# Performance work log

Hardware: AMD Instinct MI355X
Metric: run time of the kernel (lower is better)

## Reference

```python
import jax, jax.numpy as jnp
import numpy as np

N = 262144      # total nodes
E = 1048576     # total edges
G = 8192        # num graphs (= batch[-1]+1)
H = 128         # hidden
L = 4           # layers
VA = 64         # atom feature vocab
VB = 8          # bond feature vocab
FA = 9          # atom feature columns
FB = 3          # bond feature columns
BN_EPS = 1e-5


def _bn(x, g, b, m, v):
    # BatchNorm1d in eval mode: running stats
    return (x - m) * jax.lax.rsqrt(v + BN_EPS) * g + b


def setup_inputs() -> dict:
    key = jax.random.key(0)
    ks = jax.random.split(key, 40)
    rn = lambda k, s, sc=0.05: jax.random.normal(k, s, dtype=jnp.float32) * sc
    x = jax.random.randint(ks[0], (N, FA), 0, VA)
    edge_index = jax.random.randint(ks[1], (2, E), 0, N)
    edge_attr = jax.random.randint(ks[2], (E, FB), 0, VB)
    batch = jnp.sort(jax.random.randint(ks[3], (N,), 0, G))
    batch = batch.at[0].set(0).at[-1].set(G - 1)
    params = dict(
        atom_emb=rn(ks[4], (FA, VA, H)),
        vn_emb=rn(ks[5], (H,)),
        bond_emb=rn(ks[6], (L, FB, VB, H)),
        conv_eps=rn(ks[7], (L,)),
        conv_W1=rn(ks[8], (L, H, 2 * H)), conv_b1=rn(ks[9], (L, 2 * H)),
        conv_bn_g=1.0 + rn(ks[10], (L, 2 * H)), conv_bn_b=rn(ks[11], (L, 2 * H)),
        conv_bn_m=rn(ks[12], (L, 2 * H), 0.1),
        conv_bn_v=0.5 + jax.random.uniform(ks[13], (L, 2 * H)) * 0.5,
        conv_W2=rn(ks[14], (L, 2 * H, H)), conv_b2=rn(ks[15], (L, H)),
        vn1_W=rn(ks[16], (L, 2 * H, 2 * H)), vn1_b=rn(ks[17], (L, 2 * H)),
        vn1_g=1.0 + rn(ks[18], (L, 2 * H)), vn1_be=rn(ks[19], (L, 2 * H)),
        vn1_m=rn(ks[20], (L, 2 * H), 0.1),
        vn1_v=0.5 + jax.random.uniform(ks[21], (L, 2 * H)) * 0.5,
        vn2_W=rn(ks[22], (L, 2 * H, H)), vn2_b=rn(ks[23], (L, H)),
        vn2_g=1.0 + rn(ks[24], (L, H)), vn2_be=rn(ks[25], (L, H)),
        vn2_m=rn(ks[26], (L, H), 0.1),
        vn2_v=0.5 + jax.random.uniform(ks[27], (L, H)) * 0.5,
        pW1=rn(ks[28], (H, H)), pb1=rn(ks[29], (H,)),
        pW2=rn(ks[30], (H, 1)), pb2=rn(ks[31], (1,)),
    )
    return dict(x=x, edge_index=edge_index, edge_attr=edge_attr, batch=batch, **params)


def reference(x, edge_index, edge_attr, batch, atom_emb, vn_emb, bond_emb,
              conv_eps, conv_W1, conv_b1, conv_bn_g, conv_bn_b, conv_bn_m, conv_bn_v,
              conv_W2, conv_b2, vn1_W, vn1_b, vn1_g, vn1_be, vn1_m, vn1_v,
              vn2_W, vn2_b, vn2_g, vn2_be, vn2_m, vn2_v, pW1, pb1, pW2, pb2):
    src, dst = edge_index[0], edge_index[1]
    # AtomEncoder: sum of per-feature embeddings -> [N, H]
    h = atom_emb[jnp.arange(FA)[:, None], x.T].sum(0)
    # virtual node embedding broadcast to all graphs: [G, H]
    vn = jnp.broadcast_to(vn_emb, (G, H))
    for i in range(L):
        h = h + vn[batch]
        # CombConv (GIN-with-edge-features): msg = relu(x_j + bond_emb)
        e = bond_emb[i][jnp.arange(FB)[:, None], edge_attr.T].sum(0)  # [E, H]
        msg = jax.nn.relu(h[src] + e)
        agg = jax.ops.segment_sum(msg, dst, num_segments=N)  # [N, H]
        z = (1.0 + conv_eps[i]) * h + agg
        z = jax.nn.relu(_bn(z @ conv_W1[i] + conv_b1[i],
                            conv_bn_g[i], conv_bn_b[i], conv_bn_m[i], conv_bn_v[i]))
        h = z @ conv_W2[i] + conv_b2[i]
        # virtual node update: gather-concat-MLP, pool, MLP
        t = jnp.concatenate([vn[batch], h], axis=-1)  # [N, 2H]
        t = jax.nn.relu(_bn(t @ vn1_W[i] + vn1_b[i],
                            vn1_g[i], vn1_be[i], vn1_m[i], vn1_v[i]))
        pooled = jax.ops.segment_sum(t, batch, num_segments=G)  # [G, 2H]
        vn = jax.nn.relu(_bn(pooled @ vn2_W[i] + vn2_b[i],
                             vn2_g[i], vn2_be[i], vn2_m[i], vn2_v[i]))
    # JK='L': last virtual-node representation; dropout=0
    out = jax.nn.relu(vn @ pW1 + pb1) @ pW2 + pb2  # [G, 1]
    return jnp.clip(out, 0.0, 50.0)  # eval-mode clamp
```

## Files before the change

kernel.cpp:

```cpp
#include <hip/hip_runtime.h>
#include <hip/hip_fp16.h>

#define NN 262144
#define EE 1048576
#define GG 8192
#define HH 128
#define FBc 3
#define VAc 64
#define VBc 8
#define FAc 9

typedef _Float16 f16;
typedef _Float16 f16x8 __attribute__((ext_vector_type(8)));
typedef float f32x4 __attribute__((ext_vector_type(4)));

__device__ __forceinline__ float h2f(ushort u) {
    __half h; *(ushort*)&h = u; return __half2float(h);
}
__device__ __forceinline__ ushort f2h(float f) {
    __half h = __float2half_rn(f); return *(ushort*)&h;
}

__global__ void k_zero(float* __restrict__ p) {
    size_t i = (size_t)(blockIdx.x * 256 + threadIdx.x) * 4;
    *(float4*)(p + i) = make_float4(0.f, 0.f, 0.f, 0.f);
}

__global__ void k_atom(const int* __restrict__ x, const float* __restrict__ emb,
                       float* __restrict__ h) {
    int t = blockIdx.x * 256 + threadIdx.x;
    int n = t >> 5, c = (t & 31) << 2;
    if (n >= NN) return;
    float4 a = make_float4(0.f, 0.f, 0.f, 0.f);
#pragma unroll
    for (int f = 0; f < FAc; ++f) {
        int v = x[n * FAc + f];
        float4 e = *(const float4*)(emb + ((size_t)(f * VAc + v)) * HH + c);
        a.x += e.x; a.y += e.y; a.z += e.z; a.w += e.w;
    }
    *(float4*)(h + (size_t)n * HH + c) = a;
}

__global__ void k_init_vn(const float* __restrict__ vn_emb, float* __restrict__ vn) {
    int t = blockIdx.x * 256 + threadIdx.x;
    int g = t >> 5, c = (t & 31) << 2;
    *(float4*)(vn + (size_t)g * HH + c) = *(const float4*)(vn_emb + c);
}

__global__ void k_hist(const int* __restrict__ ei, int* __restrict__ deg) {
    int e = blockIdx.x * 256 + threadIdx.x;
    atomicAdd(&deg[ei[EE + e]], 1);
}
__global__ void k_scan1(const int* __restrict__ deg, int* __restrict__ rowptr,
                        int* __restrict__ sums) {
    __shared__ int s[256];
    int base = blockIdx.x * 1024 + threadIdx.x * 4;
    int4 d = *(const int4*)(deg + base);
    int t = d.x + d.y + d.z + d.w;
    s[threadIdx.x] = t;
    __syncthreads();
    for (int off = 1; off < 256; off <<= 1) {
        int v = (threadIdx.x >= off) ? s[threadIdx.x - off] : 0;
        __syncthreads();
        s[threadIdx.x] += v;
        __syncthreads();
    }
    int excl = s[threadIdx.x] - t;
    int4 o; o.x = excl; o.y = excl + d.x; o.z = o.y + d.y; o.w = o.z + d.z;
    *(int4*)(rowptr + base) = o;
    if (threadIdx.x == 255) sums[blockIdx.x] = s[255];
}
__global__ void k_scan2(int* __restrict__ sums) {
    __shared__ int s[256];
    int t = sums[threadIdx.x];
    s[threadIdx.x] = t;
    __syncthreads();
    for (int off = 1; off < 256; off <<= 1) {
        int v = (threadIdx.x >= off) ? s[threadIdx.x - off] : 0;
        __syncthreads();
        s[threadIdx.x] += v;
        __syncthreads();
    }
    sums[threadIdx.x] = s[threadIdx.x] - t;
}
__global__ void k_scan3(int* __restrict__ rowptr, const int* __restrict__ sums,
                        int* __restrict__ fill) {
    int base = blockIdx.x * 1024 + threadIdx.x * 4;
    int add = sums[blockIdx.x];
    int4 r = *(const int4*)(rowptr + base);
    r.x += add; r.y += add; r.z += add; r.w += add;
    *(int4*)(rowptr + base) = r;
    *(int4*)(fill + base) = r;
    if (blockIdx.x == 0 && threadIdx.x == 0) rowptr[NN] = EE;
}
__global__ void k_scatter(const int* __restrict__ ei, const int* __restrict__ ea,
                          int* __restrict__ fill, unsigned* __restrict__ packed) {
    int e = blockIdx.x * 256 + threadIdx.x;
    int dst = ei[EE + e];
    int pos = atomicAdd(&fill[dst], 1);
    unsigned cb = (unsigned)(ea[e * 3 + 0] + ea[e * 3 + 1] * 8 + ea[e * 3 + 2] * 64);
    packed[pos] = (unsigned)ei[e] | (cb << 18);
}

__global__ void k_ctab(const float* __restrict__ bemb, float* __restrict__ ctab) {
    int t = blockIdx.x * 256 + threadIdx.x;
    int cb = t >> 5, c = (t & 31) << 2;
    int a0 = cb & 7, a1 = (cb >> 3) & 7, a2 = cb >> 6;
    float4 b0 = *(const float4*)(bemb + (size_t)(0 * VBc + a0) * HH + c);
    float4 b1 = *(const float4*)(bemb + (size_t)(1 * VBc + a1) * HH + c);
    float4 b2 = *(const float4*)(bemb + (size_t)(2 * VBc + a2) * HH + c);
    float4 o = make_float4(b0.x + b1.x + b2.x, b0.y + b1.y + b2.y,
                           b0.z + b1.z + b2.z, b0.w + b1.w + b2.w);
    *(float4*)(ctab + (size_t)cb * HH + c) = o;
}

__global__ void k_wt(const float* __restrict__ W, ushort* __restrict__ Wt, int lk, int Nsrc) {
    int o = blockIdx.x * 256 + threadIdx.x;
    int K = 1 << lk;
    int c = o >> lk, k = o & (K - 1);
    Wt[o] = f2h(W[(size_t)k * Nsrc + c]);
}

__global__ void k_agg(const float* __restrict__ h, const float* __restrict__ vn,
                      const int* __restrict__ batch,
                      const int* __restrict__ rowptr, const unsigned* __restrict__ packed,
                      const float* __restrict__ ctab, ushort* __restrict__ agg) {
    int n = blockIdx.x * 4 + (threadIdx.x >> 6);
    int lane = threadIdx.x & 63;
    int co = lane * 2;
    int beg = rowptr[n], end = rowptr[n + 1];
    float a0 = 0.f, a1 = 0.f;
    int i = beg;
    for (; i + 1 < end; i += 2) {
        unsigned p0 = packed[i], p1 = packed[i + 1];
        int s0 = p0 & 0x3FFFF, s1 = p1 & 0x3FFFF;
        int c0 = p0 >> 18, c1 = p1 >> 18;
        float2 h0 = *(const float2*)(h + (size_t)s0 * HH + co);
        float2 h1 = *(const float2*)(h + (size_t)s1 * HH + co);
        float2 v0 = *(const float2*)(vn + (size_t)batch[s0] * HH + co);
        float2 v1 = *(const float2*)(vn + (size_t)batch[s1] * HH + co);
        float2 t0 = *(const float2*)(ctab + (size_t)c0 * HH + co);
        float2 t1 = *(const float2*)(ctab + (size_t)c1 * HH + co);
        a0 += fmaxf(h0.x + v0.x + t0.x, 0.f) + fmaxf(h1.x + v1.x + t1.x, 0.f);
        a1 += fmaxf(h0.y + v0.y + t0.y, 0.f) + fmaxf(h1.y + v1.y + t1.y, 0.f);
    }
    if (i < end) {
        unsigned p = packed[i];
        int src = p & 0x3FFFF, cb = p >> 18;
        float2 hv = *(const float2*)(h + (size_t)src * HH + co);
        float2 vv = *(const float2*)(vn + (size_t)batch[src] * HH + co);
        float2 ct = *(const float2*)(ctab + (size_t)cb * HH + co);
        a0 += fmaxf(hv.x + vv.x + ct.x, 0.f);
        a1 += fmaxf(hv.y + vv.y + ct.y, 0.f);
    }
    ushort2 o; o.x = f2h(a0 * 0.0625f); o.y = f2h(a1 * 0.0625f);
    *(ushort2*)(agg + (size_t)n * HH + co) = o;
}

__global__ void __launch_bounds__(512)
k_conv(float* __restrict__ hio, const ushort* __restrict__ agg,
       const ushort* __restrict__ W1t, const ushort* __restrict__ W2t,
       const ushort* __restrict__ W3t,
       const int* __restrict__ batch, const float* __restrict__ vn,
       const float* __restrict__ vnW,
       const float* __restrict__ eps_ptr, const float* __restrict__ b1,
       const float* __restrict__ g1v, const float* __restrict__ be1,
       const float* __restrict__ m1, const float* __restrict__ v1,
       const float* __restrict__ b2,
       const float* __restrict__ g3, const float* __restrict__ be3,
       const float* __restrict__ m3, const float* __restrict__ v3,
       float* __restrict__ pooled) {
    __shared__ ushort As[128][136];
    __shared__ ushort zs[128][264];
    __shared__ ushort Wb[128][136];
    __shared__ int batchL[128];
    float(*ts)[132] = (float(*)[132]) & zs[0][0];
    const int tid = threadIdx.x;
    const int r0 = blockIdx.x * 128;
    const int w = tid >> 6, l = tid & 63, lr = l & 15, lg = l >> 4;
    if (tid < 128) batchL[tid] = batch[r0 + tid];
    const float eps1 = 1.f + eps_ptr[0];
    __syncthreads();

    {
        int row = tid >> 2, q = tid & 3;
        const float* hp = hio + (size_t)(r0 + row) * HH + q * 32;
        const float* vp = vn + (size_t)batchL[row] * HH + q * 32;
        const ushort* ap = agg + (size_t)(r0 + row) * HH + q * 32;
#pragma unroll
        for (int j4 = 0; j4 < 4; ++j4) {
            f16x8 u = *(const f16x8*)(ap + j4 * 8);
            f16x8 o;
#pragma unroll
            for (int j = 0; j < 8; ++j) {
                float hv = hp[j4 * 8 + j] + vp[j4 * 8 + j];
                o[j] = (f16)(eps1 * hv * 0.0625f + (float)u[j]);
            }
            *(f16x8*)&As[row][q * 32 + j4 * 8] = o;
        }
    }

    for (int ch = 0; ch < 2; ++ch) {
        __syncthreads();
        {
            int c = tid >> 2, q = tid & 3;
            const ushort* wp = W1t + (size_t)(ch * 128 + c) * HH + q * 32;
#pragma unroll
            for (int j4 = 0; j4 < 4; ++j4)
                *(f16x8*)&Wb[c][q * 32 + j4 * 8] = *(const f16x8*)(wp + j4 * 8);
        }
        __syncthreads();
        f32x4 acc[8] = {};
#pragma unroll
        for (int k0 = 0; k0 < 128; k0 += 32) {
            f16x8 af = *(const f16x8*)&As[w * 16 + lr][k0 + lg * 8];
#pragma unroll
            for (int fc = 0; fc < 8; ++fc) {
                f16x8 bf = *(const f16x8*)&Wb[fc * 16 + lr][k0 + lg * 8];
                acc[fc] = __builtin_amdgcn_mfma_f32_16x16x32_f16(af, bf, acc[fc], 0, 0, 0);
            }
        }
#pragma unroll
        for (int fc = 0; fc < 8; ++fc) {
#pragma unroll
            for (int reg = 0; reg < 4; ++reg) {
                int rl = w * 16 + lg * 4 + reg;
                int col = ch * 128 + fc * 16 + lr;
                float val = acc[fc][reg] * 16.f + b1[col];
                float y = (val - m1[col]) * (g1v[col] * rsqrtf(v1[col] + 1e-5f)) + be1[col];
                zs[rl][col] = f2h(fmaxf(y, 0.f) * 0.0625f);
            }
        }
    }
    __syncthreads();

    ushort(*Wb2)[264] = (ushort(*)[264]) & Wb[0][0];
    for (int ch = 0; ch < 2; ++ch) {
        __syncthreads();
        {
            int c = tid >> 3, q = tid & 7;
            const ushort* wp = W2t + (size_t)(ch * 64 + c) * 256 + q * 32;
#pragma unroll
            for (int j4 = 0; j4 < 4; ++j4)
                *(f16x8*)&Wb2[c][q * 32 + j4 * 8] = *(const f16x8*)(wp + j4 * 8);
        }
        __syncthreads();
        f32x4 acc[4] = {};
#pragma unroll
        for (int k0 = 0; k0 < 256; k0 += 32) {
            f16x8 af = *(const f16x8*)&zs[w * 16 + lr][k0 + lg * 8];
#pragma unroll
            for (int fc = 0; fc < 4; ++fc) {
                f16x8 bf = *(const f16x8*)&Wb2[fc * 16 + lr][k0 + lg * 8];
                acc[fc] = __builtin_amdgcn_mfma_f32_16x16x32_f16(af, bf, acc[fc], 0, 0, 0);
            }
        }
#pragma unroll
        for (int fc = 0; fc < 4; ++fc) {
#pragma unroll
            for (int reg = 0; reg < 4; ++reg) {
                int rl = w * 16 + lg * 4 + reg;
                int col = ch * 64 + fc * 16 + lr;
                float hv = acc[fc][reg] * 16.f + b2[col];
                hio[(size_t)(r0 + rl) * HH + col] = hv;
                As[rl][col] = f2h(hv * 0.0625f);
            }
        }
    }

    for (int ch = 0; ch < 2; ++ch) {
        __syncthreads();
        {
            int c = tid >> 2, q = tid & 3;
            const ushort* wp = W3t + (size_t)(ch * 128 + c) * HH + q * 32;
#pragma unroll
            for (int j4 = 0; j4 < 4; ++j4)
                *(f16x8*)&Wb[c][q * 32 + j4 * 8] = *(const f16x8*)(wp + j4 * 8);
        }
        __syncthreads();
        f32x4 acc[8] = {};
#pragma unroll
        for (int k0 = 0; k0 < 128; k0 += 32) {
            f16x8 af = *(const f16x8*)&As[w * 16 + lr][k0 + lg * 8];
#pragma unroll
            for (int fc = 0; fc < 8; ++fc) {
                f16x8 bf = *(const f16x8*)&Wb[fc * 16 + lr][k0 + lg * 8];
                acc[fc] = __builtin_amdgcn_mfma_f32_16x16x32_f16(af, bf, acc[fc], 0, 0, 0);
            }
        }
#pragma unroll
        for (int fc = 0; fc < 8; ++fc) {
#pragma unroll
            for (int reg = 0; reg < 4; ++reg) {
                int rl = w * 16 + lg * 4 + reg;
                int colg = ch * 128 + fc * 16 + lr;
                int gg = batchL[rl];
                float val = acc[fc][reg] * 16.f + vnW[(size_t)gg * 256 + colg];
                float y = (val - m3[colg]) * (g3[colg] * rsqrtf(v3[colg] + 1e-5f)) + be3[colg];
                ts[rl][fc * 16 + lr] = fmaxf(y, 0.f);
            }
        }
        __syncthreads();
        {
            int col = tid & 127, rs = (tid >> 7) * 32;
            float s = 0.f;
            int cur = batchL[rs];
            for (int r = rs; r < rs + 32; ++r) {
                int gg = batchL[r];
                if (gg != cur) {
                    atomicAdd(&pooled[(size_t)cur * 256 + ch * 128 + col], s);
                    s = 0.f; cur = gg;
                }
                s += ts[r][col];
            }
            atomicAdd(&pooled[(size_t)cur * 256 + ch * 128 + col], s);
        }
    }
}

enum { E_BIAS = 0, E_BNRELU = 1 };
template <int EMODE>
__global__ void __launch_bounds__(256)
gemm_k(const void* __restrict__ Av, const float* __restrict__ B,
       const float* __restrict__ bias,
       const float* __restrict__ g_, const float* __restrict__ b_,
       const float* __restrict__ m_, const float* __restrict__ v_,
       void* __restrict__ outv, int K, int Nc) {
    __shared__ float As[64][33];
    __shared__ float Bs[32][64];
    const int tid = threadIdx.x;
    const int row0 = blockIdx.x * 64;
    const int col0 = blockIdx.y * 64;
    float acc[4][4] = {};
    const int tx = tid & 15, ty = tid >> 4;
    for (int k0 = 0; k0 < K; k0 += 32) {
#pragma unroll
        for (int p = 0; p < 2; ++p) {
            int idx = p * 256 + tid;
            {
                int r = idx >> 3, c = (idx & 7) << 2;
                size_t aoff = (size_t)(row0 + r) * K + k0 + c;
                float4 va = *(const float4*)((const float*)Av + aoff);
                As[r][c + 0] = va.x; As[r][c + 1] = va.y;
                As[r][c + 2] = va.z; As[r][c + 3] = va.w;
            }
            {
                int kr = idx >> 4, cc = (idx & 15) << 2;
                *(float4*)&Bs[kr][cc] =
                    *(const float4*)(B + (size_t)(k0 + kr) * Nc + col0 + cc);
            }
        }
        __syncthreads();
#pragma unroll
        for (int k = 0; k < 32; ++k) {
            float4 bv = *(const float4*)&Bs[k][tx << 2];
            float a0 = As[ty * 4 + 0][k];
            float a1 = As[ty * 4 + 1][k];
            float a2 = As[ty * 4 + 2][k];
            float a3 = As[ty * 4 + 3][k];
            acc[0][0] += a0 * bv.x; acc[0][1] += a0 * bv.y; acc[0][2] += a0 * bv.z; acc[0][3] += a0 * bv.w;
            acc[1][0] += a1 * bv.x; acc[1][1] += a1 * bv.y; acc[1][2] += a1 * bv.z; acc[1][3] += a1 * bv.w;
            acc[2][0] += a2 * bv.x; acc[2][1] += a2 * bv.y; acc[2][2] += a2 * bv.z; acc[2][3] += a2 * bv.w;
            acc[3][0] += a3 * bv.x; acc[3][1] += a3 * bv.y; acc[3][2] += a3 * bv.z; acc[3][3] += a3 * bv.w;
        }
        __syncthreads();
    }
#pragma unroll
    for (int j = 0; j < 4; ++j) {
        int gr = row0 + ty * 4 + j;
        float vals[4];
#pragma unroll
        for (int lx = 0; lx < 4; ++lx) {
            int gc = col0 + (tx << 2) + lx;
            float val = acc[j][lx];
            if (EMODE == E_BIAS) {
                vals[lx] = val + bias[gc];
            } else {
                float y = val + bias[gc];
                float s = g_[gc] * rsqrtf(v_[gc] + 1e-5f);
                y = (y - m_[gc]) * s + b_[gc];
                vals[lx] = fmaxf(y, 0.f);
            }
        }
        *(float4*)((float*)outv + (size_t)gr * Nc + col0 + (tx << 2)) =
            make_float4(vals[0], vals[1], vals[2], vals[3]);
    }
}

__global__ void k_final(const float* __restrict__ vn, const float* __restrict__ pW1,
                        const float* __restrict__ pb1, const float* __restrict__ pW2,
                        const float* __restrict__ pb2, float* __restrict__ out) {
    int g = blockIdx.x;
    int j = threadIdx.x;
    __shared__ float vrow[HH];
    __shared__ float red[HH];
    vrow[j] = vn[(size_t)g * HH + j];
    __syncthreads();
    float acc = pb1[j];
    for (int k = 0; k < HH; ++k) acc = fmaf(vrow[k], pW1[k * HH + j], acc);
    red[j] = fmaxf(acc, 0.f) * pW2[j];
    __syncthreads();
    for (int s = 64; s > 0; s >>= 1) {
        if (j < s) red[j] += red[j + s];
        __syncthreads();
    }
    if (j == 0) out[g] = fminf(fmaxf(red[0] + pb2[0], 0.f), 50.f);
}

extern "C" void kernel_launch(void* const* d_in, const int* in_sizes, int n_in,
                              void* d_out, int out_size, void* d_ws, size_t ws_size,
                              hipStream_t stream) {
    const int*   x        = (const int*)  d_in[0];
    const int*   ei       = (const int*)  d_in[1];
    const int*   ea       = (const int*)  d_in[2];
    const int*   batch    = (const int*)  d_in[3];
    const float* atom_emb = (const float*)d_in[4];
    const float* vn_emb   = (const float*)d_in[5];
    const float* bond_emb = (const float*)d_in[6];
    const float* conv_eps = (const float*)d_in[7];
    const float* conv_W1  = (const float*)d_in[8];
    const float* conv_b1  = (const float*)d_in[9];
    const float* cbn_g    = (const float*)d_in[10];
    const float* cbn_b    = (const float*)d_in[11];
    const float* cbn_m    = (const float*)d_in[12];
    const float* cbn_v    = (const float*)d_in[13];
    const float* conv_W2  = (const float*)d_in[14];
    const float* conv_b2  = (const float*)d_in[15];
    const float* vn1_W    = (const float*)d_in[16];
    const float* vn1_b    = (const float*)d_in[17];
    const float* vn1_g    = (const float*)d_in[18];
    const float* vn1_be   = (const float*)d_in[19];
    const float* vn1_m    = (const float*)d_in[20];
    const float* vn1_v    = (const float*)d_in[21];
    const float* vn2_W    = (const float*)d_in[22];
    const float* vn2_b    = (const float*)d_in[23];
    const float* vn2_g    = (const float*)d_in[24];
    const float* vn2_be   = (const float*)d_in[25];
    const float* vn2_m    = (const float*)d_in[26];
    const float* vn2_v    = (const float*)d_in[27];
    const float* pW1      = (const float*)d_in[28];
    const float* pb1      = (const float*)d_in[29];
    const float* pW2      = (const float*)d_in[30];
    const float* pb2      = (const float*)d_in[31];

    char* base = (char*)d_ws;
    float*    h      = (float*)base;
    ushort*   agg    = (ushort*)(base + (size_t)NN * HH * 4);
    unsigned* packed = (unsigned*)(agg + (size_t)NN * HH);
    int*      rowptr = (int*)(packed + EE);
    int*      fill   = rowptr + NN + 4;
    float*    ctab   = (float*)(fill + NN);
    int*      sums   = (int*)(ctab + 512 * HH);
    ushort*   W1t    = (ushort*)(sums + 256);
    ushort*   W2t    = W1t + 256 * 128;
    ushort*   W3t    = W2t + 128 * 256;
    float*    vn     = (float*)(W3t + 256 * 128);
    float*    vnW    = vn + (size_t)GG * HH;
    float*    pooled = vnW + (size_t)GG * 256;
    float*    out    = (float*)d_out;

    k_zero<<<256, 256, 0, stream>>>((float*)fill);
    k_hist<<<EE / 256, 256, 0, stream>>>(ei, fill);
    k_scan1<<<256, 256, 0, stream>>>(fill, rowptr, sums);
    k_scan2<<<1, 256, 0, stream>>>(sums);
    k_scan3<<<256, 256, 0, stream>>>(rowptr, sums, fill);
    k_scatter<<<EE / 256, 256, 0, stream>>>(ei, ea, fill, packed);
    k_atom<<<NN * 32 / 256, 256, 0, stream>>>(x, atom_emb, h);
    k_init_vn<<<GG * HH / 4 / 256, 256, 0, stream>>>(vn_emb, vn);

    for (int i = 0; i < 4; ++i) {
        k_ctab<<<64, 256, 0, stream>>>(bond_emb + (size_t)i * FBc * VBc * HH, ctab);
        k_agg<<<NN / 4, 256, 0, stream>>>(h, vn, batch, rowptr, packed, ctab, agg);
        k_wt<<<128, 256, 0, stream>>>(conv_W1 + (size_t)i * HH * 256, W1t, 7, 256);
        k_wt<<<128, 256, 0, stream>>>(conv_W2 + (size_t)i * 256 * HH, W2t, 8, 128);
        k_wt<<<128, 256, 0, stream>>>(vn1_W + (size_t)i * 256 * 256 + 128 * 256, W3t, 7, 256);

        {
            dim3 g3(GG / 64, 4);
            gemm_k<E_BIAS><<<g3, 256, 0, stream>>>(
                vn, vn1_W + (size_t)i * 256 * 256, vn1_b + i * 256,
                nullptr, nullptr, nullptr, nullptr, vnW, HH, 256);
        }
        k_zero<<<GG * 256 / 4 / 256, 256, 0, stream>>>(pooled);

        k_conv<<<NN / 128, 512, 0, stream>>>(
            h, agg, W1t, W2t, W3t, batch, vn, vnW, conv_eps + i,
            conv_b1 + i * 256, cbn_g + i * 256, cbn_b + i * 256,
            cbn_m + i * 256, cbn_v + i * 256, conv_b2 + i * HH,
            vn1_g + i * 256, vn1_be + i * 256, vn1_m + i * 256, vn1_v + i * 256,
            pooled);

        {
            dim3 g4(GG / 64, 2);
            gemm_k<E_BNRELU><<<g4, 256, 0, stream>>>(
                pooled, vn2_W + (size_t)i * 256 * HH, vn2_b + i * HH,
                vn2_g + i * HH, vn2_be + i * HH, vn2_m + i * HH, vn2_v + i * HH,
                vn, 256, HH);
        }
    }
    k_final<<<GG, 128, 0, stream>>>(vn, pW1, pb1, pW2, pb2, out);
}
```

Before: 1.816 ms.

## Store node features in fp16, swizzle LDS tiles, fold BN constants

Node hidden state h is now stored as pre-scaled fp16 instead of fp32. This halves the bytes read by the edge-gather aggregation and by the conv kernel. The shared-memory tiles in k_conv drop their padding in favour of an XOR swizzle, and the BatchNorm scale/shift constants are precomputed once per layer in a small prep kernel (the vn1 scale is folded into the vnW GEMM epilogue). The vn1 output is staged as fp16 in LDS so pooling happens once over all 256 columns, which cuts the synchronisations. Keeping h in fp16 between layers adds rounding error.

```diff
diff --git a/kernel.cpp b/kernel.cpp
--- a/kernel.cpp
+++ b/kernel.cpp
@@ -27,7 +27,7 @@
 }
 
 __global__ void k_atom(const int* __restrict__ x, const float* __restrict__ emb,
-                       float* __restrict__ h) {
+                       ushort* __restrict__ h16) {
     int t = blockIdx.x * 256 + threadIdx.x;
     int n = t >> 5, c = (t & 31) << 2;
     if (n >= NN) return;
@@ -38,7 +38,10 @@
         float4 e = *(const float4*)(emb + ((size_t)(f * VAc + v)) * HH + c);
         a.x += e.x; a.y += e.y; a.z += e.z; a.w += e.w;
     }
-    *(float4*)(h + (size_t)n * HH + c) = a;
+    ushort4 o;
+    o.x = f2h(a.x * 0.0625f); o.y = f2h(a.y * 0.0625f);
+    o.z = f2h(a.z * 0.0625f); o.w = f2h(a.w * 0.0625f);
+    *(ushort4*)(h16 + (size_t)n * HH + c) = o;
 }
 
 __global__ void k_init_vn(const float* __restrict__ vn_emb, float* __restrict__ vn) {
@@ -114,6 +117,24 @@
     *(float4*)(ctab + (size_t)cb * HH + c) = o;
 }
 
+__global__ void k_prep(const float* __restrict__ b1, const float* __restrict__ g1,
+                       const float* __restrict__ be1, const float* __restrict__ m1,
+                       const float* __restrict__ v1,
+                       const float* __restrict__ g3, const float* __restrict__ be3,
+                       const float* __restrict__ m3, const float* __restrict__ v3,
+                       float* __restrict__ ZA, float* __restrict__ ZB,
+                       float* __restrict__ TA, float* __restrict__ TB,
+                       float* __restrict__ S3) {
+    int c = threadIdx.x;
+    float s1 = g1[c] * rsqrtf(v1[c] + 1e-5f);
+    ZA[c] = s1;
+    ZB[c] = ((b1[c] - m1[c]) * s1 + be1[c]) * 0.0625f;
+    float s3 = g3[c] * rsqrtf(v3[c] + 1e-5f);
+    TA[c] = 16.f * s3;
+    TB[c] = be3[c] - m3[c] * s3;
+    S3[c] = s3;
+}
+
 __global__ void k_wt(const float* __restrict__ W, ushort* __restrict__ Wt, int lk, int Nsrc) {
     int o = blockIdx.x * 256 + threadIdx.x;
     int K = 1 << lk;
@@ -121,7 +142,7 @@
     Wt[o] = f2h(W[(size_t)k * Nsrc + c]);
 }
 
-__global__ void k_agg(const float* __restrict__ h, const float* __restrict__ vn,
+__global__ void k_agg(const ushort* __restrict__ h16, const float* __restrict__ vn,
                       const int* __restrict__ batch,
                       const int* __restrict__ rowptr, const unsigned* __restrict__ packed,
                       const float* __restrict__ ctab, ushort* __restrict__ agg) {
@@ -135,186 +156,207 @@
         unsigned p0 = packed[i], p1 = packed[i + 1];
         int s0 = p0 & 0x3FFFF, s1 = p1 & 0x3FFFF;
         int c0 = p0 >> 18, c1 = p1 >> 18;
-        float2 h0 = *(const float2*)(h + (size_t)s0 * HH + co);
-        float2 h1 = *(const float2*)(h + (size_t)s1 * HH + co);
+        ushort2 u0 = *(const ushort2*)(h16 + (size_t)s0 * HH + co);
+        ushort2 u1 = *(const ushort2*)(h16 + (size_t)s1 * HH + co);
         float2 v0 = *(const float2*)(vn + (size_t)batch[s0] * HH + co);
         float2 v1 = *(const float2*)(vn + (size_t)batch[s1] * HH + co);
         float2 t0 = *(const float2*)(ctab + (size_t)c0 * HH + co);
         float2 t1 = *(const float2*)(ctab + (size_t)c1 * HH + co);
-        a0 += fmaxf(h0.x + v0.x + t0.x, 0.f) + fmaxf(h1.x + v1.x + t1.x, 0.f);
-        a1 += fmaxf(h0.y + v0.y + t0.y, 0.f) + fmaxf(h1.y + v1.y + t1.y, 0.f);
+        a0 += fmaxf(16.f * h2f(u0.x) + v0.x + t0.x, 0.f)
+            + fmaxf(16.f * h2f(u1.x) + v1.x + t1.x, 0.f);
+        a1 += fmaxf(16.f * h2f(u0.y) + v0.y + t0.y, 0.f)
+            + fmaxf(16.f * h2f(u1.y) + v1.y + t1.y, 0.f);
     }
     if (i < end) {
         unsigned p = packed[i];
         int src = p & 0x3FFFF, cb = p >> 18;
-        float2 hv = *(const float2*)(h + (size_t)src * HH + co);
+        ushort2 u = *(const ushort2*)(h16 + (size_t)src * HH + co);
         float2 vv = *(const float2*)(vn + (size_t)batch[src] * HH + co);
         float2 ct = *(const float2*)(ctab + (size_t)cb * HH + co);
-        a0 += fmaxf(hv.x + vv.x + ct.x, 0.f);
-        a1 += fmaxf(hv.y + vv.y + ct.y, 0.f);
+        a0 += fmaxf(16.f * h2f(u.x) + vv.x + ct.x, 0.f);
+        a1 += fmaxf(16.f * h2f(u.y) + vv.y + ct.y, 0.f);
     }
     ushort2 o; o.x = f2h(a0 * 0.0625f); o.y = f2h(a1 * 0.0625f);
     *(ushort2*)(agg + (size_t)n * HH + co) = o;
 }
 
 __global__ void __launch_bounds__(512)
-k_conv(float* __restrict__ hio, const ushort* __restrict__ agg,
+k_conv(ushort* __restrict__ h16, const ushort* __restrict__ agg,
        const ushort* __restrict__ W1t, const ushort* __restrict__ W2t,
        const ushort* __restrict__ W3t,
        const int* __restrict__ batch, const float* __restrict__ vn,
        const float* __restrict__ vnW,
-       const float* __restrict__ eps_ptr, const float* __restrict__ b1,
-       const float* __restrict__ g1v, const float* __restrict__ be1,
-       const float* __restrict__ m1, const float* __restrict__ v1,
+       const float* __restrict__ eps_ptr,
+       const float* __restrict__ ZA, const float* __restrict__ ZB,
        const float* __restrict__ b2,
-       const float* __restrict__ g3, const float* __restrict__ be3,
-       const float* __restrict__ m3, const float* __restrict__ v3,
+       const float* __restrict__ TA, const float* __restrict__ TB,
        float* __restrict__ pooled) {
-    __shared__ ushort As[128][136];
-    __shared__ ushort zs[128][264];
-    __shared__ ushort Wb[128][136];
+    __shared__ ushort As[128][128];
+    __shared__ ushort zs[128][256];
+    __shared__ ushort Wb[128][128];
     __shared__ int batchL[128];
-    float(*ts)[132] = (float(*)[132]) & zs[0][0];
     const int tid = threadIdx.x;
     const int r0 = blockIdx.x * 128;
-    const int w = tid >> 6, l = tid & 63, lr = l & 15, lg = l >> 4;
+    const int w = tid >> 6, l = tid & 63, lr = l & 15, lg = l >> 4, lr7 = lr & 7;
     if (tid < 128) batchL[tid] = batch[r0 + tid];
     const float eps1 = 1.f + eps_ptr[0];
-    __syncthreads();
 
     {
-        int row = tid >> 2, q = tid & 3;
-        const float* hp = hio + (size_t)(r0 + row) * HH + q * 32;
-        const float* vp = vn + (size_t)batchL[row] * HH + q * 32;
-        const ushort* ap = agg + (size_t)(r0 + row) * HH + q * 32;
+        int row = w * 16 + (l >> 2), q = l & 3, r7 = row & 7;
+        int gg = batch[r0 + row];
+        const ushort* hp = h16 + (size_t)(r0 + row) * HH;
+        const float* vp = vn + (size_t)gg * HH;
+        const ushort* ap = agg + (size_t)(r0 + row) * HH;
 #pragma unroll
         for (int j4 = 0; j4 < 4; ++j4) {
-            f16x8 u = *(const f16x8*)(ap + j4 * 8);
+            int c0 = q * 32 + j4 * 8;
+            f16x8 hv = *(const f16x8*)(hp + c0);
+            float4 v0 = *(const float4*)(vp + c0);
+            float4 v1 = *(const float4*)(vp + c0 + 4);
+            f16x8 ag = *(const f16x8*)(ap + c0);
+            float vv[8] = {v0.x, v0.y, v0.z, v0.w, v1.x, v1.y, v1.z, v1.w};
             f16x8 o;
 #pragma unroll
-            for (int j = 0; j < 8; ++j) {
-                float hv = hp[j4 * 8 + j] + vp[j4 * 8 + j];
-                o[j] = (f16)(eps1 * hv * 0.0625f + (float)u[j]);
-            }
-            *(f16x8*)&As[row][q * 32 + j4 * 8] = o;
-        }
-    }
-
+            for (int j = 0; j < 8; ++j)
+                o[j] = (f16)(eps1 * ((float)hv[j] + vv[j] * 0.0625f) + (float)ag[j]);
+            *(f16x8*)&As[row][((c0 >> 3) ^ r7) << 3] = o;
+        }
+    }
+
+    f32x4 acc[8];
     for (int ch = 0; ch < 2; ++ch) {
-        __syncthreads();
+        if (ch) __syncthreads();
         {
-            int c = tid >> 2, q = tid & 3;
-            const ushort* wp = W1t + (size_t)(ch * 128 + c) * HH + q * 32;
-#pragma unroll
-            for (int j4 = 0; j4 < 4; ++j4)
-                *(f16x8*)&Wb[c][q * 32 + j4 * 8] = *(const f16x8*)(wp + j4 * 8);
-        }
-        __syncthreads();
-        f32x4 acc[8] = {};
-#pragma unroll
-        for (int k0 = 0; k0 < 128; k0 += 32) {
-            f16x8 af = *(const f16x8*)&As[w * 16 + lr][k0 + lg * 8];
+            int c = tid >> 2, q = tid & 3, c7 = c & 7;
+#pragma unroll
+            for (int j4 = 0; j4 < 4; ++j4) {
+                int blk = q * 4 + j4;
+                *(f16x8*)&Wb[c][(blk ^ c7) << 3] =
+                    *(const f16x8*)(W1t + (size_t)(ch * 128 + c) * 128 + blk * 8);
+            }
+        }
+        __syncthreads();
+#pragma unroll
+        for (int fc = 0; fc < 8; ++fc) acc[fc] = (f32x4){0.f, 0.f, 0.f, 0.f};
+#pragma unroll
+        for (int k0 = 0; k0 < 4; ++k0) {
+            int sb = ((k0 * 4 + lg) ^ lr7) << 3;
+            f16x8 af = *(const f16x8*)&As[w * 16 + lr][sb];
 #pragma unroll
             for (int fc = 0; fc < 8; ++fc) {
-                f16x8 bf = *(const f16x8*)&Wb[fc * 16 + lr][k0 + lg * 8];
+                f16x8 bf = *(const f16x8*)&Wb[fc * 16 + lr][sb];
                 acc[fc] = __builtin_amdgcn_mfma_f32_16x16x32_f16(af, bf, acc[fc], 0, 0, 0);
             }
         }
 #pragma unroll
         for (int fc = 0; fc < 8; ++fc) {
+            int col = ch * 128 + fc * 16 + lr;
+            float za = ZA[col], zb = ZB[col];
 #pragma unroll
             for (int reg = 0; reg < 4; ++reg) {
                 int rl = w * 16 + lg * 4 + reg;
-                int col = ch * 128 + fc * 16 + lr;
-                float val = acc[fc][reg] * 16.f + b1[col];
-                float y = (val - m1[col]) * (g1v[col] * rsqrtf(v1[col] + 1e-5f)) + be1[col];
-                zs[rl][col] = f2h(fmaxf(y, 0.f) * 0.0625f);
-            }
-        }
-    }
-    __syncthreads();
-
-    ushort(*Wb2)[264] = (ushort(*)[264]) & Wb[0][0];
-    for (int ch = 0; ch < 2; ++ch) {
+                float zv = fmaxf(acc[fc][reg] * za + zb, 0.f);
+                ((ushort*)zs)[rl * 256 + ((((col >> 3) ^ (rl & 7)) << 3) | (col & 7))] = f2h(zv);
+            }
+        }
+    }
+
+    for (int ch2 = 0; ch2 < 2; ++ch2) {
         __syncthreads();
         {
-            int c = tid >> 3, q = tid & 7;
-            const ushort* wp = W2t + (size_t)(ch * 64 + c) * 256 + q * 32;
-#pragma unroll
-            for (int j4 = 0; j4 < 4; ++j4)
-                *(f16x8*)&Wb2[c][q * 32 + j4 * 8] = *(const f16x8*)(wp + j4 * 8);
-        }
-        __syncthreads();
-        f32x4 acc[4] = {};
-#pragma unroll
-        for (int k0 = 0; k0 < 256; k0 += 32) {
-            f16x8 af = *(const f16x8*)&zs[w * 16 + lr][k0 + lg * 8];
+            int c = tid >> 3, q = tid & 7, c7 = c & 7;
+#pragma unroll
+            for (int j4 = 0; j4 < 4; ++j4) {
+                int blk = q * 4 + j4;
+                *(f16x8*)((ushort*)Wb + c * 256 + ((blk ^ c7) << 3)) =
+                    *(const f16x8*)(W2t + (size_t)(ch2 * 64 + c) * 256 + blk * 8);
+            }
+        }
+        __syncthreads();
+#pragma unroll
+        for (int fc = 0; fc < 4; ++fc) acc[fc] = (f32x4){0.f, 0.f, 0.f, 0.f};
+#pragma unroll
+        for (int k0 = 0; k0 < 8; ++k0) {
+            int sb = ((k0 * 4 + lg) ^ lr7) << 3;
+            f16x8 af = *(const f16x8*)&zs[w * 16 + lr][sb];
 #pragma unroll
             for (int fc = 0; fc < 4; ++fc) {
-                f16x8 bf = *(const f16x8*)&Wb2[fc * 16 + lr][k0 + lg * 8];
+                f16x8 bf = *(const f16x8*)((ushort*)Wb + (fc * 16 + lr) * 256 + sb);
                 acc[fc] = __builtin_amdgcn_mfma_f32_16x16x32_f16(af, bf, acc[fc], 0, 0, 0);
             }
         }
 #pragma unroll
         for (int fc = 0; fc < 4; ++fc) {
+            int col = ch2 * 64 + fc * 16 + lr;
+            float bb = b2[col];
 #pragma unroll
             for (int reg = 0; reg < 4; ++reg) {
                 int rl = w * 16 + lg * 4 + reg;
-                int col = ch * 64 + fc * 16 + lr;
-                float hv = acc[fc][reg] * 16.f + b2[col];
-                hio[(size_t)(r0 + rl) * HH + col] = hv;
-                As[rl][col] = f2h(hv * 0.0625f);
-            }
-        }
-    }
-
-    for (int ch = 0; ch < 2; ++ch) {
+                float hv = acc[fc][reg] * 16.f + bb;
+                ushort hq = f2h(hv * 0.0625f);
+                h16[(size_t)(r0 + rl) * HH + col] = hq;
+                As[rl][(((col >> 3) ^ (rl & 7)) << 3) | (col & 7)] = hq;
+            }
+        }
+    }
+
+    for (int ch3 = 0; ch3 < 2; ++ch3) {
         __syncthreads();
         {
-            int c = tid >> 2, q = tid & 3;
-            const ushort* wp = W3t + (size_t)(ch * 128 + c) * HH + q * 32;
-#pragma unroll
-            for (int j4 = 0; j4 < 4; ++j4)
-                *(f16x8*)&Wb[c][q * 32 + j4 * 8] = *(const f16x8*)(wp + j4 * 8);
-        }
-        __syncthreads();
-        f32x4 acc[8] = {};
-#pragma unroll
-        for (int k0 = 0; k0 < 128; k0 += 32) {
-            f16x8 af = *(const f16x8*)&As[w * 16 + lr][k0 + lg * 8];
+            int c = tid >> 2, q = tid & 3, c7 = c & 7;
+#pragma unroll
+            for (int j4 = 0; j4 < 4; ++j4) {
+                int blk = q * 4 + j4;
+                *(f16x8*)&Wb[c][(blk ^ c7) << 3] =
+                    *(const f16x8*)(W3t + (size_t)(ch3 * 128 + c) * 128 + blk * 8);
+            }
+        }
+        __syncthreads();
+#pragma unroll
+        for (int fc = 0; fc < 8; ++fc) acc[fc] = (f32x4){0.f, 0.f, 0.f, 0.f};
+#pragma unroll
+        for (int k0 = 0; k0 < 4; ++k0) {
+            int sb = ((k0 * 4 + lg) ^ lr7) << 3;
+            f16x8 af = *(const f16x8*)&As[w * 16 + lr][sb];
 #pragma unroll
             for (int fc = 0; fc < 8; ++fc) {
-                f16x8 bf = *(const f16x8*)&Wb[fc * 16 + lr][k0 + lg * 8];
+                f16x8 bf = *(const f16x8*)&Wb[fc * 16 + lr][sb];
                 acc[fc] = __builtin_amdgcn_mfma_f32_16x16x32_f16(af, bf, acc[fc], 0, 0, 0);
             }
         }
+        const float* vp[4];
+        int rls[4];
+#pragma unroll
+        for (int reg = 0; reg < 4; ++reg) {
+            rls[reg] = w * 16 + lg * 4 + reg;
+            vp[reg] = vnW + (size_t)batchL[rls[reg]] * 256;
+        }
 #pragma unroll
         for (int fc = 0; fc < 8; ++fc) {
+            int colg = ch3 * 128 + fc * 16 + lr;
+            float ta = TA[colg], tb = TB[colg];
 #pragma unroll
             for (int reg = 0; reg < 4; ++reg) {
-                int rl = w * 16 + lg * 4 + reg;
-                int colg = ch * 128 + fc * 16 + lr;
-                int gg = batchL[rl];
-                float val = acc[fc][reg] * 16.f + vnW[(size_t)gg * 256 + colg];
-                float y = (val - m3[colg]) * (g3[colg] * rsqrtf(v3[colg] + 1e-5f)) + be3[colg];
-                ts[rl][fc * 16 + lr] = fmaxf(y, 0.f);
-            }
-        }
-        __syncthreads();
-        {
-            int col = tid & 127, rs = (tid >> 7) * 32;
-            float s = 0.f;
-            int cur = batchL[rs];
-            for (int r = rs; r < rs + 32; ++r) {
-                int gg = batchL[r];
-                if (gg != cur) {
-                    atomicAdd(&pooled[(size_t)cur * 256 + ch * 128 + col], s);
-                    s = 0.f; cur = gg;
-                }
-                s += ts[r][col];
-            }
-            atomicAdd(&pooled[(size_t)cur * 256 + ch * 128 + col], s);
-        }
+                int rl = rls[reg];
+                float tv = fmaxf(acc[fc][reg] * ta + vp[reg][colg] + tb, 0.f);
+                ((ushort*)zs)[rl * 256 + ((((colg >> 3) ^ (rl & 7)) << 3) | (colg & 7))] = f2h(tv);
+            }
+        }
+    }
+    __syncthreads();
+    {
+        int col = tid & 255, rs = (tid >> 8) * 64;
+        float s = 0.f;
+        int cur = batchL[rs];
+        for (int r = rs; r < rs + 64; ++r) {
+            int gg = batchL[r];
+            if (gg != cur) {
+                atomicAdd(&pooled[(size_t)cur * 256 + col], s);
+                s = 0.f; cur = gg;
+            }
+            s += h2f(((const ushort*)zs)[r * 256 + ((((col >> 3) ^ (r & 7)) << 3) | (col & 7))]);
+        }
+        atomicAdd(&pooled[(size_t)cur * 256 + col], s);
     }
 }
 
@@ -325,6 +367,7 @@
        const float* __restrict__ bias,
        const float* __restrict__ g_, const float* __restrict__ b_,
        const float* __restrict__ m_, const float* __restrict__ v_,
+       const float* __restrict__ scp,
        void* __restrict__ outv, int K, int Nc) {
     __shared__ float As[64][33];
     __shared__ float Bs[32][64];
@@ -374,7 +417,9 @@
             int gc = col0 + (tx << 2) + lx;
             float val = acc[j][lx];
             if (EMODE == E_BIAS) {
-                vals[lx] = val + bias[gc];
+                float v = val + bias[gc];
+                if (scp) v *= scp[gc];
+                vals[lx] = v;
             } else {
                 float y = val + bias[gc];
                 float s = g_[gc] * rsqrtf(v_[gc] + 1e-5f);
@@ -444,8 +489,8 @@
     const float* pb2      = (const float*)d_in[31];
 
     char* base = (char*)d_ws;
-    float*    h      = (float*)base;
-    ushort*   agg    = (ushort*)(base + (size_t)NN * HH * 4);
+    ushort*   h16    = (ushort*)base;
+    ushort*   agg    = h16 + (size_t)NN * HH;
     unsigned* packed = (unsigned*)(agg + (size_t)NN * HH);
     int*      rowptr = (int*)(packed + EE);
     int*      fill   = rowptr + NN + 4;
@@ -454,7 +499,12 @@
     ushort*   W1t    = (ushort*)(sums + 256);
     ushort*   W2t    = W1t + 256 * 128;
     ushort*   W3t    = W2t + 128 * 256;
-    float*    vn     = (float*)(W3t + 256 * 128);
+    float*    ZA     = (float*)(W3t + 256 * 128);
+    float*    ZB     = ZA + 256;
+    float*    TA     = ZB + 256;
+    float*    TB     = TA + 256;
+    float*    S3     = TB + 256;
+    float*    vn     = S3 + 256;
     float*    vnW    = vn + (size_t)GG * HH;
     float*    pooled = vnW + (size_t)GG * 256;
     float*    out    = (float*)d_out;
@@ -465,37 +515,40 @@
     k_scan2<<<1, 256, 0, stream>>>(sums);
     k_scan3<<<256, 256, 0, stream>>>(rowptr, sums, fill);
     k_scatter<<<EE / 256, 256, 0, stream>>>(ei, ea, fill, packed);
-    k_atom<<<NN * 32 / 256, 256, 0, stream>>>(x, atom_emb, h);
+    k_atom<<<NN * 32 / 256, 256, 0, stream>>>(x, atom_emb, h16);
     k_init_vn<<<GG * HH / 4 / 256, 256, 0, stream>>>(vn_emb, vn);
 
     for (int i = 0; i < 4; ++i) {
         k_ctab<<<64, 256, 0, stream>>>(bond_emb + (size_t)i * FBc * VBc * HH, ctab);
-        k_agg<<<NN / 4, 256, 0, stream>>>(h, vn, batch, rowptr, packed, ctab, agg);
+        k_prep<<<1, 256, 0, stream>>>(
+            conv_b1 + i * 256, cbn_g + i * 256, cbn_b + i * 256,
+            cbn_m + i * 256, cbn_v + i * 256,
+            vn1_g + i * 256, vn1_be + i * 256, vn1_m + i * 256, vn1_v + i * 256,
+            ZA, ZB, TA, TB, S3);
         k_wt<<<128, 256, 0, stream>>>(conv_W1 + (size_t)i * HH * 256, W1t, 7, 256);
         k_wt<<<128, 256, 0, stream>>>(conv_W2 + (size_t)i * 256 * HH, W2t, 8, 128);
         k_wt<<<128, 256, 0, stream>>>(vn1_W + (size_t)i * 256 * 256 + 128 * 256, W3t, 7, 256);
+
+        k_agg<<<NN / 4, 256, 0, stream>>>(h16, vn, batch, rowptr, packed, ctab, agg);
 
         {
             dim3 g3(GG / 64, 4);
             gemm_k<E_BIAS><<<g3, 256, 0, stream>>>(
                 vn, vn1_W + (size_t)i * 256 * 256, vn1_b + i * 256,
-                nullptr, nullptr, nullptr, nullptr, vnW, HH, 256);
+                nullptr, nullptr, nullptr, nullptr, S3, vnW, HH, 256);
         }
         k_zero<<<GG * 256 / 4 / 256, 256, 0, stream>>>(pooled);
 
         k_conv<<<NN / 128, 512, 0, stream>>>(
-            h, agg, W1t, W2t, W3t, batch, vn, vnW, conv_eps + i,
-            conv_b1 + i * 256, cbn_g + i * 256, cbn_b + i * 256,
-            cbn_m + i * 256, cbn_v + i * 256, conv_b2 + i * HH,
-            vn1_g + i * 256, vn1_be + i * 256, vn1_m + i * 256, vn1_v + i * 256,
-            pooled);
+            h16, agg, W1t, W2t, W3t, batch, vn, vnW, conv_eps + i,
+            ZA, ZB, conv_b2 + i * HH, TA, TB, pooled);
 
         {
             dim3 g4(GG / 64, 2);
             gemm_k<E_BNRELU><<<g4, 256, 0, stream>>>(
                 pooled, vn2_W + (size_t)i * 256 * HH, vn2_b + i * HH,
                 vn2_g + i * HH, vn2_be + i * HH, vn2_m + i * HH, vn2_v + i * HH,
-                vn, 256, HH);
+                nullptr, vn, 256, HH);
         }
     }
     k_final<<<GG, 128, 0, stream>>>(vn, pW1, pb1, pW2, pb2, out);
```

After: 1.703 ms. -6.2%, faster.
